# Optimization experiments

Measured on AMD Instinct MI355X. Metric: run time of the kernel, lower is better.

## Reference

```python
import jax, jax.numpy as jnp
import numpy as np

B, H, I = 131072, 128, 128  # batch, hidden_size, input_size (must be equal per source math)


def setup_inputs() -> dict:
    key = jax.random.key(0)
    ks = jax.random.split(key, 7)
    return {
        "x":   jax.random.normal(ks[0], (B, H), dtype=jnp.float32),
        "h_0": jax.random.normal(ks[1], (B, H), dtype=jnp.float32),
        "c_0": jax.random.normal(ks[2], (B, H), dtype=jnp.float32),
        "ih":  jax.random.normal(ks[3], (4 * H, I), dtype=jnp.float32) * 0.1,
        "hh":  jax.random.normal(ks[4], (4 * H, H), dtype=jnp.float32) * 0.1,
        "ib":  jax.random.normal(ks[5], (4 * H,), dtype=jnp.float32) * 0.1,
        "hb":  jax.random.normal(ks[6], (4 * H,), dtype=jnp.float32) * 0.1,
    }


def reference(x, h_0, c_0, ih, hh, ib, hb):
    hidden = hh.shape[1]
    # torch.split(ih, H) -> 4 chunks [H, I]; gate = x @ chunk (note: NOT chunk.T)
    ih4 = ih.reshape(4, hidden, -1)        # [4, H, I]
    hh4 = hh.reshape(4, hidden, hidden)    # [4, H, H]
    ib4 = ib.reshape(4, 1, hidden)
    hb4 = hb.reshape(4, 1, hidden)
    # combined gate GEMM: gates[g] = x @ ih4[g] + ib4[g] + h_0 @ hh4[g] + hb4[g]
    gates = (jnp.einsum('bh,ghi->gbi', x, ih4)
             + jnp.einsum('bh,ghk->gbk', h_0, hh4)
             + ib4 + hb4)                  # [4, B, H]
    I_g, F_g, G_g, O_g = gates[0], gates[1], gates[2], gates[3]
    c_1 = c_0 * jax.nn.sigmoid(F_g) + jax.nn.sigmoid(I_g) * jnp.tanh(G_g)
    h_1 = jax.nn.sigmoid(O_g) + jnp.tanh(c_1)  # faithful to source (additive, not gated)
    return (h_1, c_1, I_g, F_g, G_g, O_g)
```

## Files before the change

kernel.cpp:

```cpp
#include <hip/hip_runtime.h>
#include <hip/hip_bf16.h>

typedef __attribute__((ext_vector_type(8))) short short8;
typedef __attribute__((ext_vector_type(4))) float f32x4;

#define HSZ 128
#define BM  32
#define NT  512

#define LGKM_BARRIER() asm volatile("s_waitcnt lgkmcnt(0)\n\ts_barrier" ::: "memory")

__device__ __forceinline__ unsigned short f2bf(float f) {
    union { float f; unsigned int u; } c; c.f = f;
    return (unsigned short)((c.u + 0x7FFFu + ((c.u >> 16) & 1u)) >> 16);
}

__global__ void prep_kernel(const float* __restrict__ ih, const float* __restrict__ hh,
                            const float* __restrict__ ib, const float* __restrict__ hb,
                            unsigned short* __restrict__ Wp, float* __restrict__ bias) {
    int tid = blockIdx.x * blockDim.x + threadIdx.x;
    int col = tid >> 5;
    int kg  = tid & 31;
    int g = col >> 7, i = col & 127;
    short8 pk;
    #pragma unroll
    for (int j = 0; j < 8; ++j) {
        int k = kg * 8 + j;
        float v = (k < HSZ) ? ih[(g * HSZ + k) * HSZ + i]
                            : hh[(g * HSZ + (k - HSZ)) * HSZ + i];
        pk[j] = (short)f2bf(v);
    }
    *reinterpret_cast<short8*>(Wp + col * 256 + kg * 8) = pk;
    if (kg == 0) bias[col] = ib[col] + hb[col];
}

union SMem {
    unsigned short A[BM * 264];
    f32x4 T[2][BM * 32];
};

__global__ __launch_bounds__(NT, 6)
void lstm_kernel(const float* __restrict__ x, const float* __restrict__ h0,
                 const float* __restrict__ c0,
                 const unsigned short* __restrict__ Wp,
                 const float* __restrict__ biasp,
                 float* __restrict__ out, long BH) {
    constexpr int PITCH = 264;
    __shared__ SMem sm;

    const int t = threadIdx.x;
    const long rowBase = (long)blockIdx.x * BM;

    {
        const float4* x4 = reinterpret_cast<const float4*>(x + rowBase * HSZ);
        const float4* h4 = reinterpret_cast<const float4*>(h0 + rowBase * HSZ);
        #pragma unroll
        for (int j = 0; j < 2; ++j) {
            int fi = t + j * NT;
            int row = fi >> 5;
            int c4  = fi & 31;
            float4 vx = x4[fi];
            float4 vh = h4[fi];
            ushort4 px; px.x = f2bf(vx.x); px.y = f2bf(vx.y); px.z = f2bf(vx.z); px.w = f2bf(vx.w);
            ushort4 ph; ph.x = f2bf(vh.x); ph.y = f2bf(vh.y); ph.z = f2bf(vh.z); ph.w = f2bf(vh.w);
            *reinterpret_cast<ushort4*>(&sm.A[row * PITCH + c4 * 4]) = px;
            *reinterpret_cast<ushort4*>(&sm.A[row * PITCH + HSZ + c4 * 4]) = ph;
        }
    }
    LGKM_BARRIER();

    const int lane = t & 63;
    const int wid  = t >> 6;
    const int wn = wid;
    const int lr = lane & 15;
    const int lk = lane >> 4;

    const char* Ab = reinterpret_cast<const char*>(sm.A) + lr * (PITCH * 2) + lk * 16;
    const char* Wb = reinterpret_cast<const char*>(Wp) + (wn * 16 + lr) * 512 + lk * 16;

    f32x4 acc[2][4] = {};

    #pragma unroll
    for (int ks = 0; ks < 8; ++ks) {
        short8 a0 = *reinterpret_cast<const short8*>(Ab + ks * 64);
        short8 a1 = *reinterpret_cast<const short8*>(Ab + 16 * (PITCH * 2) + ks * 64);
        #pragma unroll
        for (int g = 0; g < 4; ++g) {
            short8 w = *reinterpret_cast<const short8*>(Wb + (g * 128) * 512 + ks * 64);
            acc[0][g] = __builtin_amdgcn_mfma_f32_16x16x32_bf16(w, a0, acc[0][g], 0, 0, 0);
            acc[1][g] = __builtin_amdgcn_mfma_f32_16x16x32_bf16(w, a1, acc[1][g], 0, 0, 0);
        }
    }

    f32x4 c0v[2];
    #pragma unroll
    for (int mi = 0; mi < 2; ++mi) {
        long pos = (rowBase + mi * 16 + lr) * HSZ + wn * 16 + lk * 4;
        c0v[mi] = *reinterpret_cast<const f32x4*>(c0 + pos);
    }

    #pragma unroll
    for (int g = 0; g < 4; ++g) {
        f32x4 bg = *reinterpret_cast<const f32x4*>(biasp + g * HSZ + wn * 16 + lk * 4);
        acc[0][g] += bg;
        acc[1][g] += bg;
    }

    LGKM_BARRIER();

    #define SIDX(MI) ((MI * 16 + lr) * 32 + ((wn * 4 + lk) ^ (lr & 7)))

    auto flush = [&](const f32x4* T, long obase) {
        #pragma unroll
        for (int p = 0; p < 2; ++p) {
            int f = t + p * NT;
            int row = f >> 5, c = f & 31;
            f32x4 v = T[row * 32 + (c ^ (row & 7))];
            __builtin_nontemporal_store(v,
                reinterpret_cast<f32x4*>(out + obase + (rowBase + row) * (long)HSZ + c * 4));
        }
    };

    #pragma unroll
    for (int mi = 0; mi < 2; ++mi) sm.T[0][SIDX(mi)] = acc[mi][0];
    LGKM_BARRIER();

    flush(sm.T[0], 2 * BH);
    #pragma unroll
    for (int mi = 0; mi < 2; ++mi) sm.T[1][SIDX(mi)] = acc[mi][1];
    LGKM_BARRIER();

    flush(sm.T[1], 3 * BH);
    #pragma unroll
    for (int mi = 0; mi < 2; ++mi) sm.T[0][SIDX(mi)] = acc[mi][2];
    LGKM_BARRIER();

    flush(sm.T[0], 4 * BH);
    #pragma unroll
    for (int mi = 0; mi < 2; ++mi) sm.T[1][SIDX(mi)] = acc[mi][3];
    LGKM_BARRIER();

    flush(sm.T[1], 5 * BH);
    #pragma unroll
    for (int mi = 0; mi < 2; ++mi) {
        f32x4 v;
        #pragma unroll
        for (int r = 0; r < 4; ++r) {
            float iv = acc[mi][0][r];
            float fv = acc[mi][1][r];
            float gv = acc[mi][2][r];
            float si = 1.f / (1.f + __expf(-iv));
            float sf = 1.f / (1.f + __expf(-fv));
            float tg = 1.f - 2.f / (__expf(2.f * gv) + 1.f);
            v[r] = c0v[mi][r] * sf + si * tg;
        }
        sm.T[0][SIDX(mi)] = v;
    }
    LGKM_BARRIER();

    flush(sm.T[0], BH);
    #pragma unroll
    for (int mi = 0; mi < 2; ++mi) {
        f32x4 c1 = sm.T[0][SIDX(mi)];
        f32x4 v;
        #pragma unroll
        for (int r = 0; r < 4; ++r) {
            float ov = acc[mi][3][r];
            float so = 1.f / (1.f + __expf(-ov));
            float th = 1.f - 2.f / (__expf(2.f * c1[r]) + 1.f);
            v[r] = so + th;
        }
        sm.T[1][SIDX(mi)] = v;
    }
    LGKM_BARRIER();

    flush(sm.T[1], 0);
    #undef SIDX
}

extern "C" void kernel_launch(void* const* d_in, const int* in_sizes, int n_in,
                              void* d_out, int out_size, void* d_ws, size_t ws_size,
                              hipStream_t stream) {
    const float* x  = (const float*)d_in[0];
    const float* h0 = (const float*)d_in[1];
    const float* c0 = (const float*)d_in[2];
    const float* ih = (const float*)d_in[3];
    const float* hh = (const float*)d_in[4];
    const float* ib = (const float*)d_in[5];
    const float* hb = (const float*)d_in[6];
    float* out = (float*)d_out;

    unsigned short* Wp = (unsigned short*)d_ws;
    float* bias = (float*)((char*)d_ws + 512 * 256 * 2);

    long BH = in_sizes[2];
    long B  = BH / HSZ;

    prep_kernel<<<64, 256, 0, stream>>>(ih, hh, ib, hb, Wp, bias);
    lstm_kernel<<<(int)(B / BM), NT, 0, stream>>>(x, h0, c0, Wp, bias, out, BH);
}
```

Measured before the change: 189.8 us.

## Make LSTM kernel persistent with register prefetch of next tile inputs

Replaces the one-block-per-tile launch with a fixed grid of 768 persistent blocks that loop over batch tiles. While the current tile finishes its epilogue, each block prefetches the next tile's x and h0 into registers, and bias loads are hoisted out of the loop. The aim is to hide global load latency and cut block launch overhead. The cost is higher register pressure, and shared memory is no longer a union, so LDS use grows, which may lower occupancy.

```diff
diff --git a/kernel.cpp b/kernel.cpp
--- a/kernel.cpp
+++ b/kernel.cpp
@@ -7,6 +7,7 @@
 #define HSZ 128
 #define BM  32
 #define NT  512
+#define GRID 768
 
 #define LGKM_BARRIER() asm volatile("s_waitcnt lgkmcnt(0)\n\ts_barrier" ::: "memory")
 
@@ -34,148 +35,158 @@
     if (kg == 0) bias[col] = ib[col] + hb[col];
 }
 
-union SMem {
-    unsigned short A[BM * 264];
-    f32x4 T[2][BM * 32];
-};
-
 __global__ __launch_bounds__(NT, 6)
 void lstm_kernel(const float* __restrict__ x, const float* __restrict__ h0,
                  const float* __restrict__ c0,
                  const unsigned short* __restrict__ Wp,
                  const float* __restrict__ biasp,
-                 float* __restrict__ out, long BH) {
+                 float* __restrict__ out, long BH, int ntiles) {
     constexpr int PITCH = 264;
-    __shared__ SMem sm;
+    __shared__ unsigned short A_lds[BM * PITCH];
+    __shared__ f32x4 T[2][BM * 32];
 
     const int t = threadIdx.x;
-    const long rowBase = (long)blockIdx.x * BM;
-
-    {
-        const float4* x4 = reinterpret_cast<const float4*>(x + rowBase * HSZ);
-        const float4* h4 = reinterpret_cast<const float4*>(h0 + rowBase * HSZ);
-        #pragma unroll
-        for (int j = 0; j < 2; ++j) {
-            int fi = t + j * NT;
-            int row = fi >> 5;
-            int c4  = fi & 31;
-            float4 vx = x4[fi];
-            float4 vh = h4[fi];
-            ushort4 px; px.x = f2bf(vx.x); px.y = f2bf(vx.y); px.z = f2bf(vx.z); px.w = f2bf(vx.w);
-            ushort4 ph; ph.x = f2bf(vh.x); ph.y = f2bf(vh.y); ph.z = f2bf(vh.z); ph.w = f2bf(vh.w);
-            *reinterpret_cast<ushort4*>(&sm.A[row * PITCH + c4 * 4]) = px;
-            *reinterpret_cast<ushort4*>(&sm.A[row * PITCH + HSZ + c4 * 4]) = ph;
-        }
-    }
-    LGKM_BARRIER();
-
     const int lane = t & 63;
     const int wid  = t >> 6;
     const int wn = wid;
     const int lr = lane & 15;
     const int lk = lane >> 4;
 
-    const char* Ab = reinterpret_cast<const char*>(sm.A) + lr * (PITCH * 2) + lk * 16;
+    const int fi0 = t;
+    const int fi1 = t + NT;
+
+    int tile = blockIdx.x;
+    f32x4 sx0, sx1, sh0, sh1;
+    {
+        const f32x4* x4 = reinterpret_cast<const f32x4*>(x + (long)tile * BM * HSZ);
+        const f32x4* h4 = reinterpret_cast<const f32x4*>(h0 + (long)tile * BM * HSZ);
+        sx0 = x4[fi0]; sx1 = x4[fi1];
+        sh0 = h4[fi0]; sh1 = h4[fi1];
+    }
+
+    f32x4 bg[4];
+    #pragma unroll
+    for (int g = 0; g < 4; ++g)
+        bg[g] = *reinterpret_cast<const f32x4*>(biasp + g * HSZ + wn * 16 + lk * 4);
+
     const char* Wb = reinterpret_cast<const char*>(Wp) + (wn * 16 + lr) * 512 + lk * 16;
-
-    f32x4 acc[2][4] = {};
-
-    #pragma unroll
-    for (int ks = 0; ks < 8; ++ks) {
-        short8 a0 = *reinterpret_cast<const short8*>(Ab + ks * 64);
-        short8 a1 = *reinterpret_cast<const short8*>(Ab + 16 * (PITCH * 2) + ks * 64);
-        #pragma unroll
-        for (int g = 0; g < 4; ++g) {
-            short8 w = *reinterpret_cast<const short8*>(Wb + (g * 128) * 512 + ks * 64);
-            acc[0][g] = __builtin_amdgcn_mfma_f32_16x16x32_bf16(w, a0, acc[0][g], 0, 0, 0);
-            acc[1][g] = __builtin_amdgcn_mfma_f32_16x16x32_bf16(w, a1, acc[1][g], 0, 0, 0);
-        }
+    const char* Ab = reinterpret_cast<const char*>(A_lds) + lr * (PITCH * 2) + lk * 16;
+
+    while (tile < ntiles) {
+        const long rowBase = (long)tile * BM;
+
+        {
+            int row0 = fi0 >> 5, c40 = fi0 & 31;
+            int row1 = fi1 >> 5, c41 = fi1 & 31;
+            ushort4 p;
+            p.x = f2bf(sx0.x); p.y = f2bf(sx0.y); p.z = f2bf(sx0.z); p.w = f2bf(sx0.w);
+            *reinterpret_cast<ushort4*>(&A_lds[row0 * PITCH + c40 * 4]) = p;
+            p.x = f2bf(sx1.x); p.y = f2bf(sx1.y); p.z = f2bf(sx1.z); p.w = f2bf(sx1.w);
+            *reinterpret_cast<ushort4*>(&A_lds[row1 * PITCH + c41 * 4]) = p;
+            p.x = f2bf(sh0.x); p.y = f2bf(sh0.y); p.z = f2bf(sh0.z); p.w = f2bf(sh0.w);
+            *reinterpret_cast<ushort4*>(&A_lds[row0 * PITCH + HSZ + c40 * 4]) = p;
+            p.x = f2bf(sh1.x); p.y = f2bf(sh1.y); p.z = f2bf(sh1.z); p.w = f2bf(sh1.w);
+            *reinterpret_cast<ushort4*>(&A_lds[row1 * PITCH + HSZ + c41 * 4]) = p;
+        }
+        LGKM_BARRIER();
+
+        f32x4 acc[2][4] = {};
+        #pragma unroll
+        for (int ks = 0; ks < 8; ++ks) {
+            short8 a0 = *reinterpret_cast<const short8*>(Ab + ks * 64);
+            short8 a1 = *reinterpret_cast<const short8*>(Ab + 16 * (PITCH * 2) + ks * 64);
+            #pragma unroll
+            for (int g = 0; g < 4; ++g) {
+                short8 w = *reinterpret_cast<const short8*>(Wb + (g * 128) * 512 + ks * 64);
+                acc[0][g] = __builtin_amdgcn_mfma_f32_16x16x32_bf16(w, a0, acc[0][g], 0, 0, 0);
+                acc[1][g] = __builtin_amdgcn_mfma_f32_16x16x32_bf16(w, a1, acc[1][g], 0, 0, 0);
+            }
+        }
+
+        f32x4 c0v[2];
+        #pragma unroll
+        for (int mi = 0; mi < 2; ++mi) {
+            long pos = (rowBase + mi * 16 + lr) * HSZ + wn * 16 + lk * 4;
+            c0v[mi] = *reinterpret_cast<const f32x4*>(c0 + pos);
+        }
+
+        #pragma unroll
+        for (int g = 0; g < 4; ++g) { acc[0][g] += bg[g]; acc[1][g] += bg[g]; }
+
+        int ntile = tile + GRID;
+        if (ntile < ntiles) {
+            const f32x4* x4 = reinterpret_cast<const f32x4*>(x + (long)ntile * BM * HSZ);
+            const f32x4* h4 = reinterpret_cast<const f32x4*>(h0 + (long)ntile * BM * HSZ);
+            sx0 = x4[fi0]; sx1 = x4[fi1];
+            sh0 = h4[fi0]; sh1 = h4[fi1];
+        }
+
+        LGKM_BARRIER();
+
+        #define SIDX(MI) ((MI * 16 + lr) * 32 + ((wn * 4 + lk) ^ (lr & 7)))
+        auto flush = [&](const f32x4* Tb, long obase) {
+            #pragma unroll
+            for (int p = 0; p < 2; ++p) {
+                int f = t + p * NT;
+                int row = f >> 5, c = f & 31;
+                f32x4 v = Tb[row * 32 + (c ^ (row & 7))];
+                __builtin_nontemporal_store(v,
+                    reinterpret_cast<f32x4*>(out + obase + (rowBase + row) * (long)HSZ + c * 4));
+            }
+        };
+
+        #pragma unroll
+        for (int mi = 0; mi < 2; ++mi) T[0][SIDX(mi)] = acc[mi][0];
+        LGKM_BARRIER();
+        flush(T[0], 2 * BH);
+        #pragma unroll
+        for (int mi = 0; mi < 2; ++mi) T[1][SIDX(mi)] = acc[mi][1];
+        LGKM_BARRIER();
+        flush(T[1], 3 * BH);
+        #pragma unroll
+        for (int mi = 0; mi < 2; ++mi) T[0][SIDX(mi)] = acc[mi][2];
+        LGKM_BARRIER();
+        flush(T[0], 4 * BH);
+        #pragma unroll
+        for (int mi = 0; mi < 2; ++mi) T[1][SIDX(mi)] = acc[mi][3];
+        LGKM_BARRIER();
+        flush(T[1], 5 * BH);
+        #pragma unroll
+        for (int mi = 0; mi < 2; ++mi) {
+            f32x4 v;
+            #pragma unroll
+            for (int r = 0; r < 4; ++r) {
+                float iv = acc[mi][0][r];
+                float fv = acc[mi][1][r];
+                float gv = acc[mi][2][r];
+                float si = 1.f / (1.f + __expf(-iv));
+                float sf = 1.f / (1.f + __expf(-fv));
+                float tg = 1.f - 2.f / (__expf(2.f * gv) + 1.f);
+                v[r] = c0v[mi][r] * sf + si * tg;
+            }
+            T[0][SIDX(mi)] = v;
+        }
+        LGKM_BARRIER();
+        flush(T[0], BH);
+        #pragma unroll
+        for (int mi = 0; mi < 2; ++mi) {
+            f32x4 c1 = T[0][SIDX(mi)];
+            f32x4 v;
+            #pragma unroll
+            for (int r = 0; r < 4; ++r) {
+                float ov = acc[mi][3][r];
+                float so = 1.f / (1.f + __expf(-ov));
+                float th = 1.f - 2.f / (__expf(2.f * c1[r]) + 1.f);
+                v[r] = so + th;
+            }
+            T[1][SIDX(mi)] = v;
+        }
+        LGKM_BARRIER();
+        flush(T[1], 0);
+        #undef SIDX
+
+        tile = ntile;
     }
-
-    f32x4 c0v[2];
-    #pragma unroll
-    for (int mi = 0; mi < 2; ++mi) {
-        long pos = (rowBase + mi * 16 + lr) * HSZ + wn * 16 + lk * 4;
-        c0v[mi] = *reinterpret_cast<const f32x4*>(c0 + pos);
-    }
-
-    #pragma unroll
-    for (int g = 0; g < 4; ++g) {
-        f32x4 bg = *reinterpret_cast<const f32x4*>(biasp + g * HSZ + wn * 16 + lk * 4);
-        acc[0][g] += bg;
-        acc[1][g] += bg;
-    }
-
-    LGKM_BARRIER();
-
-    #define SIDX(MI) ((MI * 16 + lr) * 32 + ((wn * 4 + lk) ^ (lr & 7)))
-
-    auto flush = [&](const f32x4* T, long obase) {
-        #pragma unroll
-        for (int p = 0; p < 2; ++p) {
-            int f = t + p * NT;
-            int row = f >> 5, c = f & 31;
-            f32x4 v = T[row * 32 + (c ^ (row & 7))];
-            __builtin_nontemporal_store(v,
-                reinterpret_cast<f32x4*>(out + obase + (rowBase + row) * (long)HSZ + c * 4));
-        }
-    };
-
-    #pragma unroll
-    for (int mi = 0; mi < 2; ++mi) sm.T[0][SIDX(mi)] = acc[mi][0];
-    LGKM_BARRIER();
-
-    flush(sm.T[0], 2 * BH);
-    #pragma unroll
-    for (int mi = 0; mi < 2; ++mi) sm.T[1][SIDX(mi)] = acc[mi][1];
-    LGKM_BARRIER();
-
-    flush(sm.T[1], 3 * BH);
-    #pragma unroll
-    for (int mi = 0; mi < 2; ++mi) sm.T[0][SIDX(mi)] = acc[mi][2];
-    LGKM_BARRIER();
-
-    flush(sm.T[0], 4 * BH);
-    #pragma unroll
-    for (int mi = 0; mi < 2; ++mi) sm.T[1][SIDX(mi)] = acc[mi][3];
-    LGKM_BARRIER();
-
-    flush(sm.T[1], 5 * BH);
-    #pragma unroll
-    for (int mi = 0; mi < 2; ++mi) {
-        f32x4 v;
-        #pragma unroll
-        for (int r = 0; r < 4; ++r) {
-            float iv = acc[mi][0][r];
-            float fv = acc[mi][1][r];
-            float gv = acc[mi][2][r];
-            float si = 1.f / (1.f + __expf(-iv));
-            float sf = 1.f / (1.f + __expf(-fv));
-            float tg = 1.f - 2.f / (__expf(2.f * gv) + 1.f);
-            v[r] = c0v[mi][r] * sf + si * tg;
-        }
-        sm.T[0][SIDX(mi)] = v;
-    }
-    LGKM_BARRIER();
-
-    flush(sm.T[0], BH);
-    #pragma unroll
-    for (int mi = 0; mi < 2; ++mi) {
-        f32x4 c1 = sm.T[0][SIDX(mi)];
-        f32x4 v;
-        #pragma unroll
-        for (int r = 0; r < 4; ++r) {
-            float ov = acc[mi][3][r];
-            float so = 1.f / (1.f + __expf(-ov));
-            float th = 1.f - 2.f / (__expf(2.f * c1[r]) + 1.f);
-            v[r] = so + th;
-        }
-        sm.T[1][SIDX(mi)] = v;
-    }
-    LGKM_BARRIER();
-
-    flush(sm.T[1], 0);
-    #undef SIDX
 }
 
 extern "C" void kernel_launch(void* const* d_in, const int* in_sizes, int n_in,
@@ -194,8 +205,8 @@
     float* bias = (float*)((char*)d_ws + 512 * 256 * 2);
 
     long BH = in_sizes[2];
-    long B  = BH / HSZ;
+    int ntiles = (int)(BH / HSZ / BM);
 
     prep_kernel<<<64, 256, 0, stream>>>(ih, hh, ib, hb, Wp, bias);
-    lstm_kernel<<<(int)(B / BM), NT, 0, stream>>>(x, h0, c0, Wp, bias, out, BH);
-}
+    lstm_kernel<<<GRID, NT, 0, stream>>>(x, h0, c0, Wp, bias, out, BH, ntiles);
+}
```

After: 364.6 us. 92.2% more time.

## Double threads per block and split row tiles across waves

Applied to the files above, without the earlier changes.

Raises the block size from 512 to 1024 threads so each of the 16 waves computes one 16-row by 16-column tile for all four gates, instead of 8 waves each covering two row tiles. This halves per-thread registers and work and adds more waves in flight to hide memory latency. In exchange, each wave now loads its weight fragments separately, so global weight traffic per block doubles, and barrier cost grows with the larger block. The launch-bounds occupancy hint changes to 8.

```diff
diff --git a/kernel.cpp b/kernel.cpp
--- a/kernel.cpp
+++ b/kernel.cpp
@@ -6,7 +6,7 @@
 
 #define HSZ 128
 #define BM  32
-#define NT  512
+#define NT  1024
 
 #define LGKM_BARRIER() asm volatile("s_waitcnt lgkmcnt(0)\n\ts_barrier" ::: "memory")
 
@@ -39,7 +39,7 @@
     f32x4 T[2][BM * 32];
 };
 
-__global__ __launch_bounds__(NT, 6)
+__global__ __launch_bounds__(NT, 8)
 void lstm_kernel(const float* __restrict__ x, const float* __restrict__ h0,
                  const float* __restrict__ c0,
                  const unsigned short* __restrict__ Wp,
@@ -54,128 +54,103 @@
     {
         const float4* x4 = reinterpret_cast<const float4*>(x + rowBase * HSZ);
         const float4* h4 = reinterpret_cast<const float4*>(h0 + rowBase * HSZ);
-        #pragma unroll
-        for (int j = 0; j < 2; ++j) {
-            int fi = t + j * NT;
-            int row = fi >> 5;
-            int c4  = fi & 31;
-            float4 vx = x4[fi];
-            float4 vh = h4[fi];
-            ushort4 px; px.x = f2bf(vx.x); px.y = f2bf(vx.y); px.z = f2bf(vx.z); px.w = f2bf(vx.w);
-            ushort4 ph; ph.x = f2bf(vh.x); ph.y = f2bf(vh.y); ph.z = f2bf(vh.z); ph.w = f2bf(vh.w);
-            *reinterpret_cast<ushort4*>(&sm.A[row * PITCH + c4 * 4]) = px;
-            *reinterpret_cast<ushort4*>(&sm.A[row * PITCH + HSZ + c4 * 4]) = ph;
-        }
+        int row = t >> 5;
+        int c4  = t & 31;
+        float4 vx = x4[t];
+        float4 vh = h4[t];
+        ushort4 px; px.x = f2bf(vx.x); px.y = f2bf(vx.y); px.z = f2bf(vx.z); px.w = f2bf(vx.w);
+        ushort4 ph; ph.x = f2bf(vh.x); ph.y = f2bf(vh.y); ph.z = f2bf(vh.z); ph.w = f2bf(vh.w);
+        *reinterpret_cast<ushort4*>(&sm.A[row * PITCH + c4 * 4]) = px;
+        *reinterpret_cast<ushort4*>(&sm.A[row * PITCH + HSZ + c4 * 4]) = ph;
     }
     LGKM_BARRIER();
 
     const int lane = t & 63;
     const int wid  = t >> 6;
-    const int wn = wid;
+    const int wm = wid & 1;
+    const int ws = wid >> 1;
     const int lr = lane & 15;
     const int lk = lane >> 4;
 
-    const char* Ab = reinterpret_cast<const char*>(sm.A) + lr * (PITCH * 2) + lk * 16;
-    const char* Wb = reinterpret_cast<const char*>(Wp) + (wn * 16 + lr) * 512 + lk * 16;
+    const char* Ab = reinterpret_cast<const char*>(sm.A)
+                   + (wm * 16 + lr) * (PITCH * 2) + lk * 16;
+    const char* Wb = reinterpret_cast<const char*>(Wp) + (ws * 16 + lr) * 512 + lk * 16;
 
-    f32x4 acc[2][4] = {};
+    f32x4 acc[4] = {};
 
     #pragma unroll
     for (int ks = 0; ks < 8; ++ks) {
         short8 a0 = *reinterpret_cast<const short8*>(Ab + ks * 64);
-        short8 a1 = *reinterpret_cast<const short8*>(Ab + 16 * (PITCH * 2) + ks * 64);
         #pragma unroll
         for (int g = 0; g < 4; ++g) {
             short8 w = *reinterpret_cast<const short8*>(Wb + (g * 128) * 512 + ks * 64);
-            acc[0][g] = __builtin_amdgcn_mfma_f32_16x16x32_bf16(w, a0, acc[0][g], 0, 0, 0);
-            acc[1][g] = __builtin_amdgcn_mfma_f32_16x16x32_bf16(w, a1, acc[1][g], 0, 0, 0);
+            acc[g] = __builtin_amdgcn_mfma_f32_16x16x32_bf16(w, a0, acc[g], 0, 0, 0);
         }
     }
 
-    f32x4 c0v[2];
-    #pragma unroll
-    for (int mi = 0; mi < 2; ++mi) {
-        long pos = (rowBase + mi * 16 + lr) * HSZ + wn * 16 + lk * 4;
-        c0v[mi] = *reinterpret_cast<const f32x4*>(c0 + pos);
+    f32x4 c0v;
+    {
+        long pos = (rowBase + wm * 16 + lr) * HSZ + ws * 16 + lk * 4;
+        c0v = *reinterpret_cast<const f32x4*>(c0 + pos);
     }
 
     #pragma unroll
-    for (int g = 0; g < 4; ++g) {
-        f32x4 bg = *reinterpret_cast<const f32x4*>(biasp + g * HSZ + wn * 16 + lk * 4);
-        acc[0][g] += bg;
-        acc[1][g] += bg;
-    }
+    for (int g = 0; g < 4; ++g)
+        acc[g] += *reinterpret_cast<const f32x4*>(biasp + g * HSZ + ws * 16 + lk * 4);
 
     LGKM_BARRIER();
 
-    #define SIDX(MI) ((MI * 16 + lr) * 32 + ((wn * 4 + lk) ^ (lr & 7)))
+    const int sidx = (wm * 16 + lr) * 32 + ((ws * 4 + lk) ^ ((wm * 16 + lr) & 7));
 
-    auto flush = [&](const f32x4* T, long obase) {
-        #pragma unroll
-        for (int p = 0; p < 2; ++p) {
-            int f = t + p * NT;
-            int row = f >> 5, c = f & 31;
-            f32x4 v = T[row * 32 + (c ^ (row & 7))];
-            __builtin_nontemporal_store(v,
-                reinterpret_cast<f32x4*>(out + obase + (rowBase + row) * (long)HSZ + c * 4));
-        }
+    auto flush = [&](const f32x4* Tb, long obase) {
+        int row = t >> 5, c = t & 31;
+        f32x4 v = Tb[row * 32 + (c ^ (row & 7))];
+        __builtin_nontemporal_store(v,
+            reinterpret_cast<f32x4*>(out + obase + (rowBase + row) * (long)HSZ + c * 4));
     };
 
-    #pragma unroll
-    for (int mi = 0; mi < 2; ++mi) sm.T[0][SIDX(mi)] = acc[mi][0];
+    sm.T[0][sidx] = acc[0];
     LGKM_BARRIER();
-
     flush(sm.T[0], 2 * BH);
-    #pragma unroll
-    for (int mi = 0; mi < 2; ++mi) sm.T[1][SIDX(mi)] = acc[mi][1];
+    sm.T[1][sidx] = acc[1];
     LGKM_BARRIER();
-
     flush(sm.T[1], 3 * BH);
-    #pragma unroll
-    for (int mi = 0; mi < 2; ++mi) sm.T[0][SIDX(mi)] = acc[mi][2];
+    sm.T[0][sidx] = acc[2];
     LGKM_BARRIER();
-
     flush(sm.T[0], 4 * BH);
-    #pragma unroll
-    for (int mi = 0; mi < 2; ++mi) sm.T[1][SIDX(mi)] = acc[mi][3];
+    sm.T[1][sidx] = acc[3];
     LGKM_BARRIER();
-
     flush(sm.T[1], 5 * BH);
-    #pragma unroll
-    for (int mi = 0; mi < 2; ++mi) {
+    {
         f32x4 v;
         #pragma unroll
         for (int r = 0; r < 4; ++r) {
-            float iv = acc[mi][0][r];
-            float fv = acc[mi][1][r];
-            float gv = acc[mi][2][r];
+            float iv = acc[0][r];
+            float fv = acc[1][r];
+            float gv = acc[2][r];
             float si = 1.f / (1.f + __expf(-iv));
             float sf = 1.f / (1.f + __expf(-fv));
             float tg = 1.f - 2.f / (__expf(2.f * gv) + 1.f);
-            v[r] = c0v[mi][r] * sf + si * tg;
+            v[r] = c0v[r] * sf + si * tg;
         }
-        sm.T[0][SIDX(mi)] = v;
+        sm.T[0][sidx] = v;
     }
     LGKM_BARRIER();
-
     flush(sm.T[0], BH);
-    #pragma unroll
-    for (int mi = 0; mi < 2; ++mi) {
-        f32x4 c1 = sm.T[0][SIDX(mi)];
+    {
+        f32x4 c1 = sm.T[0][sidx];
         f32x4 v;
         #pragma unroll
         for (int r = 0; r < 4; ++r) {
-            float ov = acc[mi][3][r];
+            float ov = acc[3][r];
             float so = 1.f / (1.f + __expf(-ov));
             float th = 1.f - 2.f / (__expf(2.f * c1[r]) + 1.f);
             v[r] = so + th;
         }
-        sm.T[1][SIDX(mi)] = v;
+        sm.T[1][sidx] = v;
     }
     LGKM_BARRIER();
-
     flush(sm.T[1], 0);
-    #undef SIDX
 }
 
 extern "C" void kernel_launch(void* const* d_in, const int* in_sizes, int n_in,
```

After: 306.6 us. 61.6% more time.
